# Performance work log

Hardware: AMD Instinct MI355X
Metric: run time of the kernel (lower is better)

The kernel has to match this reference:

```python
import jax, jax.numpy as jnp
import numpy as np

HEAD_SIZE = 64

def setup_inputs() -> dict:
    key = jax.random.key(0)
    k1, k2, k3 = jax.random.split(key, 3)
    B, T, C = 4, 4096, 1024
    x = jax.random.normal(k1, (B, T, C), dtype=jnp.float32)
    # nn.Linear(C, head_size, bias=False); stored as [in, out] so x @ W matches x @ weight.T
    Wk = jax.random.normal(k2, (C, HEAD_SIZE), dtype=jnp.float32) * (C ** -0.5)
    Wv = jax.random.normal(k3, (C, HEAD_SIZE), dtype=jnp.float32) * (C ** -0.5)
    return {"x": x, "Wk": Wk, "Wv": Wv}

def reference(x, Wk, Wv):
    # Faithful to source: q = self.key(x)  (query projection is unused -> Q == K)
    B, T, C = x.shape
    k = jnp.einsum('btc,ch->bth', x, Wk)           # [B,T,H]
    q = jnp.einsum('btc,ch->bth', x, Wk)           # same projection (source bug)
    scores = jnp.einsum('bth,bsh->bts', q, k) * (HEAD_SIZE ** -0.5)  # [B,T,T]
    causal = jnp.tril(jnp.ones((T, T), dtype=bool))
    scores = jnp.where(causal, scores, -jnp.inf)
    weights = jax.nn.softmax(scores, axis=-1)      # dropout p=0 (eval) -> identity
    v = jnp.einsum('btc,ch->bth', x, Wv)
    out = jnp.einsum('bts,bsh->bth', weights, v)   # [B,T,H]
    return out
```

## Files before the change

### kernel.cpp

```cpp
#include <hip/hip_runtime.h>

typedef short bf16x8 __attribute__((ext_vector_type(8)));
typedef float f32x4 __attribute__((ext_vector_type(4)));
typedef float f32x16 __attribute__((ext_vector_type(16)));
typedef unsigned u32x4v __attribute__((ext_vector_type(4)));

#define T_SEQ 4096
#define CDIM  1024
#define HD    64
#define NROWS 16384

__device__ inline float exp2fast(float x) {
  return __builtin_amdgcn_exp2f(x);
}

__device__ inline unsigned short f2bf(float f) {
  unsigned u = __builtin_bit_cast(unsigned, f);
  u = (u + 0x7fffu + ((u >> 16) & 1u)) >> 16;
  return (unsigned short)u;
}
__device__ inline unsigned cvt_pk_bf16(float lo, float hi) {
  unsigned r;
  asm("v_cvt_pk_bf16_f32 %0, %1, %2" : "=v"(r) : "v"(lo), "v"(hi));
  return r;
}
__device__ inline float bf2f(unsigned short u) {
  unsigned v = (unsigned)u << 16;
  return __builtin_bit_cast(float, v);
}
__device__ inline void gload_lds16(const unsigned short* g, unsigned char* l) {
  __builtin_amdgcn_global_load_lds(
      (const __attribute__((address_space(1))) unsigned int*)(const void*)g,
      (__attribute__((address_space(3))) unsigned int*)(void*)l, 16, 0, 0);
}

__global__ __launch_bounds__(256) void prep_w(
    const float* __restrict__ Wk, const float* __restrict__ Wv,
    unsigned short* __restrict__ Wt) {
  __shared__ float tile[64][68];
  const int t = threadIdx.x;
  const int mat = blockIdx.x & 1;
  const int k0 = (blockIdx.x >> 1) * 64;
  const float* W = mat ? Wv : Wk;
  #pragma unroll
  for (int pp = 0; pp < 4; ++pp) {
    int idx = t + 256 * pp, row = idx >> 4, c4 = idx & 15;
    float4 v = *(const float4*)&W[(size_t)(k0 + row) * HD + c4 * 4];
    *(float4*)&tile[row][c4 * 4] = v;
  }
  __syncthreads();
  #pragma unroll
  for (int j = 0; j < 2; ++j) {
    int n = t & 63, j8 = (t >> 6) + 4 * j;
    unsigned ow[4];
    #pragma unroll
    for (int w = 0; w < 4; ++w)
      ow[w] = cvt_pk_bf16(tile[j8 * 8 + 2 * w][n], tile[j8 * 8 + 2 * w + 1][n]);
    u32x4v ov = {ow[0], ow[1], ow[2], ow[3]};
    *(u32x4v*)&Wt[(size_t)(mat * 64 + n) * CDIM + k0 + j8 * 8] = ov;
  }
}

__global__ __launch_bounds__(256) void proj_mfma(
    const float* __restrict__ x, const unsigned short* __restrict__ Wt,
    unsigned short* __restrict__ Kb, unsigned short* __restrict__ Vb) {
  __shared__ __align__(16) unsigned char xsb[16384];
  __shared__ __align__(16) unsigned char wsb[65536];
  const int tid = threadIdx.x;
  const int lane = tid & 63, wave = tid >> 6;
  const int wm = wave & 1, wn = wave >> 1;
  const int lg = lane >> 4, lc = lane & 15;
  const int row0 = blockIdx.x * 64;

  float4 xreg[8];
  auto load_x = [&](int kk) {
    #pragma unroll
    for (int p = 0; p < 8; ++p) {
      int idx = tid + 256 * p, r = idx >> 5, c4 = idx & 31;
      xreg[p] = *(const float4*)&x[(size_t)(row0 + r) * CDIM + kk + c4 * 4];
    }
  };
  auto write_x = [&]() {
    #pragma unroll
    for (int p = 0; p < 8; ++p) {
      int idx = tid + 256 * p, r = idx >> 5, c4 = idx & 31;
      uint2 v;
      v.x = cvt_pk_bf16(xreg[p].x, xreg[p].y);
      v.y = cvt_pk_bf16(xreg[p].z, xreg[p].w);
      int byt = (r * 256 + c4 * 8) ^ ((r & 7) << 4);
      *(uint2*)(xsb + byt) = v;
    }
  };
  auto gload_W = [&](int kk, int buf) {
    unsigned char* wb = wsb + buf * 32768;
    #pragma unroll
    for (int p = 0; p < 8; ++p) {
      int ci = p * 256 + tid;
      int r = ci >> 4;
      int c8 = (ci & 15) ^ (r & 7);
      gload_lds16(&Wt[(size_t)r * CDIM + kk + c8 * 8],
                  wb + (p * 256 + wave * 64) * 16);
    }
  };

  f32x4 acc[2][4];
  #pragma unroll
  for (int mf = 0; mf < 2; ++mf)
    #pragma unroll
    for (int nf = 0; nf < 4; ++nf) acc[mf][nf] = (f32x4){0.f, 0.f, 0.f, 0.f};

  gload_W(0, 0);
  load_x(0);
  for (int kk = 0; kk < CDIM; kk += 128) {
    const int cur = (kk >> 7) & 1;
    __syncthreads();
    write_x();
    __syncthreads();
    if (kk + 128 < CDIM) { gload_W(kk + 128, cur ^ 1); load_x(kk + 128); }
    const unsigned char* wb = wsb + cur * 32768;
    #pragma unroll
    for (int dd = 0; dd < 4; ++dd) {
      bf16x8 a[2], bfr[4];
      #pragma unroll
      for (int mf = 0; mf < 2; ++mf) {
        int r = wm * 32 + mf * 16 + lc;
        int sw = (r & 7) << 4;
        a[mf] = *(const bf16x8*)(xsb + ((r * 256 + dd * 64 + lg * 16) ^ sw));
      }
      #pragma unroll
      for (int nf = 0; nf < 4; ++nf) {
        int r = wn * 64 + nf * 16 + lc;
        int sw = (r & 7) << 4;
        bfr[nf] = *(const bf16x8*)(wb + ((r * 256 + dd * 64 + lg * 16) ^ sw));
      }
      __builtin_amdgcn_s_setprio(1);
      #pragma unroll
      for (int mf = 0; mf < 2; ++mf)
        #pragma unroll
        for (int nf = 0; nf < 4; ++nf)
          acc[mf][nf] = __builtin_amdgcn_mfma_f32_16x16x32_bf16(a[mf], bfr[nf], acc[mf][nf], 0, 0, 0);
      __builtin_amdgcn_s_setprio(0);
    }
  }

  unsigned short* Ob = (wn == 0) ? Kb : Vb;
  #pragma unroll
  for (int mf = 0; mf < 2; ++mf)
    #pragma unroll
    for (int r = 0; r < 4; ++r) {
      int rg = row0 + wm * 32 + mf * 16 + lg * 4 + r;
      #pragma unroll
      for (int nf = 0; nf < 4; ++nf)
        Ob[(size_t)rg * HD + nf * 16 + lc] = f2bf(acc[mf][nf][r]);
    }
}

__global__ __launch_bounds__(512) void attn_part(
    const unsigned short* __restrict__ Kb, const unsigned short* __restrict__ Vb,
    unsigned short* __restrict__ Opart, float* __restrict__ Ml) {
  __shared__ __align__(16) unsigned char lds[32768];

  const int tid = threadIdx.x;
  const int lane = tid & 63;
  const int wq = tid >> 6;
  const int hi = lane >> 5;
  const int lq = lane & 31;

  const int b = blockIdx.x & 3;
  int qb = 0, c = 0;
  {
    int u = blockIdx.x >> 2, acc = 0;
    for (int q = 15; q >= 0; --q) {
      int nch = q + 1;
      if (u < acc + nch) { qb = q; c = u - acc; break; }
      acc += nch;
    }
  }
  const int kstart = c * 256;
  const int q0g = qb * 256 + wq * 32;
  const int qg = q0g + lq;
  const size_t base = (size_t)b * T_SEQ;
  const float SCALE2 = 0.18033688011112042f;

  bf16x8 qf[4];
  {
    const unsigned short* qp = &Kb[(base + q0g + lq) * HD];
    #pragma unroll
    for (int dd = 0; dd < 4; ++dd) {
      bf16x8 t = *(const bf16x8*)&qp[dd * 16 + hi * 8];
      const unsigned short* ts = (const unsigned short*)&t;
      unsigned ow[4];
      #pragma unroll
      for (int w = 0; w < 4; ++w)
        ow[w] = cvt_pk_bf16(bf2f(ts[2 * w]) * SCALE2, bf2f(ts[2 * w + 1]) * SCALE2);
      u32x4v ov = {ow[0], ow[1], ow[2], ow[3]};
      qf[dd] = __builtin_bit_cast(bf16x8, ov);
    }
  }

  f32x16 oT0, oT1;
  #pragma unroll
  for (int r = 0; r < 16; ++r) { oT0[r] = 0.f; oT1[r] = 0.f; }
  float mreg = -1e30f, lreg = 0.f;

  uint4 vreg0, vreg1;
  auto gload_K = [&](int jj, int buf) {
    const size_t kv0 = (base + kstart + (size_t)jj * 64) * HD;
    unsigned char* kb = lds + buf * 16384;
    int r = tid >> 3;
    int c8 = (tid & 7) ^ (r & 7);
    gload_lds16(&Kb[kv0 + (size_t)r * HD + c8 * 8], kb + (tid >> 6) * 1024);
  };
  auto load_v = [&](int jj) {
    if (tid < 256) {
      const size_t kv0 = (base + kstart + (size_t)jj * 64) * HD;
      int key0 = (tid & 31) * 2, d0 = (tid >> 5) * 8;
      vreg0 = *(const uint4*)&Vb[kv0 + (size_t)key0 * HD + d0];
      vreg1 = *(const uint4*)&Vb[kv0 + (size_t)(key0 + 1) * HD + d0];
    }
  };
  auto write_v = [&](int buf) {
    if (tid < 256) {
      unsigned char* vb = lds + buf * 16384 + 8192;
      int key0 = (tid & 31) * 2, d0 = (tid >> 5) * 8;
      const unsigned short* pa = (const unsigned short*)&vreg0;
      const unsigned short* pb = (const unsigned short*)&vreg1;
      #pragma unroll
      for (int j = 0; j < 8; ++j) {
        unsigned val = (unsigned)pa[j] | ((unsigned)pb[j] << 16);
        int d = d0 + j;
        int byt = (d * 128 + key0 * 2) ^ ((d & 7) << 4);
        *(unsigned*)(vb + byt) = val;
      }
    }
  };

  auto qk = [&](int buf, int ksub) -> f32x16 {
    const unsigned char* kb = lds + buf * 16384;
    f32x16 sacc;
    #pragma unroll
    for (int r = 0; r < 16; ++r) sacc[r] = 0.f;
    const int krow = ksub * 32 + lq;
    const int ksw = (krow & 7) << 4;
    #pragma unroll
    for (int dd = 0; dd < 4; ++dd) {
      bf16x8 kf = *(const bf16x8*)(kb + ((krow * 128 + dd * 32 + hi * 16) ^ ksw));
      sacc = __builtin_amdgcn_mfma_f32_32x32x16_bf16(kf, qf[dd], sacc, 0, 0, 0);
    }
    return sacc;
  };
  auto maskdiag = [&](f32x16& s, int kbase_s) {
    #pragma unroll
    for (int r = 0; r < 16; ++r) {
      int key = kbase_s + (r & 3) + 8 * (r >> 2) + 4 * hi;
      if (key > qg) s[r] = -1e38f;
    }
  };
  auto max16 = [&](const f32x16& s) -> float {
    return fmaxf(
        fmaxf(fmaxf(fmaxf(s[0], s[1]), fmaxf(s[2], s[3])),
              fmaxf(fmaxf(s[4], s[5]), fmaxf(s[6], s[7]))),
        fmaxf(fmaxf(fmaxf(s[8], s[9]), fmaxf(s[10], s[11])),
              fmaxf(fmaxf(s[12], s[13]), fmaxf(s[14], s[15]))));
  };
  auto pack2 = [&](const f32x16& s, bf16x8& p1, bf16x8& p2) {
    unsigned pk[8];
    #pragma unroll
    for (int i = 0; i < 8; ++i) pk[i] = cvt_pk_bf16(s[2 * i], s[2 * i + 1]);
    unsigned wA[4], wB[4];
    #pragma unroll
    for (int i = 0; i < 2; ++i) {
      unsigned a0 = pk[i], b0 = pk[2 + i];
      unsigned sa = (unsigned)__shfl_xor((int)a0, 32);
      unsigned sb = (unsigned)__shfl_xor((int)b0, 32);
      wA[i] = hi ? sb : a0;
      wA[2 + i] = hi ? b0 : sa;
      unsigned c0 = pk[4 + i], d0v = pk[6 + i];
      unsigned sc = (unsigned)__shfl_xor((int)c0, 32);
      unsigned sd = (unsigned)__shfl_xor((int)d0v, 32);
      wB[i] = hi ? sd : c0;
      wB[2 + i] = hi ? d0v : sc;
    }
    u32x4v t1v = {wA[0], wA[1], wA[2], wA[3]};
    u32x4v t2v = {wB[0], wB[1], wB[2], wB[3]};
    p1 = __builtin_bit_cast(bf16x8, t1v);
    p2 = __builtin_bit_cast(bf16x8, t2v);
  };
  auto pv = [&](int buf, int ksub, bf16x8 pb1, bf16x8 pb2) {
    const unsigned char* vb = lds + buf * 16384 + 8192;
    const int cb = ksub * 64;
    {
      int drow = lq;
      int swz = (drow & 7) << 4;
      bf16x8 v0 = *(const bf16x8*)(vb + ((drow * 128 + cb + hi * 16) ^ swz));
      bf16x8 v1 = *(const bf16x8*)(vb + ((drow * 128 + cb + 32 + hi * 16) ^ swz));
      oT0 = __builtin_amdgcn_mfma_f32_32x32x16_bf16(v0, pb1, oT0, 0, 0, 0);
      oT0 = __builtin_amdgcn_mfma_f32_32x32x16_bf16(v1, pb2, oT0, 0, 0, 0);
    }
    {
      int drow = 32 + lq;
      int swz = (drow & 7) << 4;
      bf16x8 v0 = *(const bf16x8*)(vb + ((drow * 128 + cb + hi * 16) ^ swz));
      bf16x8 v1 = *(const bf16x8*)(vb + ((drow * 128 + cb + 32 + hi * 16) ^ swz));
      oT1 = __builtin_amdgcn_mfma_f32_32x32x16_bf16(v0, pb1, oT1, 0, 0, 0);
      oT1 = __builtin_amdgcn_mfma_f32_32x32x16_bf16(v1, pb2, oT1, 0, 0, 0);
    }
  };

  gload_K(0, 0);
  load_v(0);
  write_v(0);
  for (int jj = 0; jj < 4; ++jj) {
    const int cur = jj & 1;
    __syncthreads();
    if (jj + 1 < 4) { gload_K(jj + 1, cur ^ 1); load_v(jj + 1); }
    const int kb0 = kstart + jj * 64;

    if (kb0 + 32 <= q0g) {
      __builtin_amdgcn_s_setprio(1);
      f32x16 s0 = qk(cur, 0);
      f32x16 s1 = qk(cur, 1);
      __builtin_amdgcn_s_setprio(0);
      if (kb0 + 32 == q0g) maskdiag(s1, kb0 + 32);
      float mx = fmaxf(max16(s0), max16(s1));
      mx = fmaxf(mx, __shfl_xor(mx, 32));
      if (!__all(mx <= mreg + 11.5f)) {
        float mn = fmaxf(mreg, mx);
        float al = exp2fast(mreg - mn);
        lreg *= al;
        #pragma unroll
        for (int r = 0; r < 16; ++r) { oT0[r] *= al; oT1[r] *= al; }
        mreg = mn;
      }
      float ps = 0.f;
      #pragma unroll
      for (int r = 0; r < 16; ++r) {
        float p0 = exp2fast(s0[r] - mreg);
        float p1 = exp2fast(s1[r] - mreg);
        ps += p0 + p1;
        s0[r] = p0;
        s1[r] = p1;
      }
      lreg += ps + __shfl_xor(ps, 32);
      bf16x8 pa1, pa2, pbb1, pbb2;
      pack2(s0, pa1, pa2);
      pack2(s1, pbb1, pbb2);
      __builtin_amdgcn_s_setprio(1);
      pv(cur, 0, pa1, pa2);
      pv(cur, 1, pbb1, pbb2);
      __builtin_amdgcn_s_setprio(0);
    } else if (kb0 <= q0g) {
      __builtin_amdgcn_s_setprio(1);
      f32x16 s0 = qk(cur, 0);
      __builtin_amdgcn_s_setprio(0);
      if (kb0 == q0g) maskdiag(s0, kb0);
      float mx = max16(s0);
      mx = fmaxf(mx, __shfl_xor(mx, 32));
      if (!__all(mx <= mreg + 11.5f)) {
        float mn = fmaxf(mreg, mx);
        float al = exp2fast(mreg - mn);
        lreg *= al;
        #pragma unroll
        for (int r = 0; r < 16; ++r) { oT0[r] *= al; oT1[r] *= al; }
        mreg = mn;
      }
      float ps = 0.f;
      #pragma unroll
      for (int r = 0; r < 16; ++r) {
        float p = exp2fast(s0[r] - mreg);
        ps += p;
        s0[r] = p;
      }
      lreg += ps + __shfl_xor(ps, 32);
      bf16x8 pa1, pa2;
      pack2(s0, pa1, pa2);
      __builtin_amdgcn_s_setprio(1);
      pv(cur, 0, pa1, pa2);
      __builtin_amdgcn_s_setprio(0);
    }

    if (jj + 1 < 4) write_v(cur ^ 1);
  }

  unsigned short* op = Opart + (size_t)blockIdx.x * 16384;
  float* mlp = Ml + (size_t)blockIdx.x * 512;
  const float invl = 1.0f / lreg;
  const int qrow = wq * 32 + lq;
  #pragma unroll
  for (int g = 0; g < 4; ++g) {
    int d0 = 8 * g + 4 * hi;
    uint2 w0, w1;
    w0.x = cvt_pk_bf16(oT0[4 * g] * invl, oT0[4 * g + 1] * invl);
    w0.y = cvt_pk_bf16(oT0[4 * g + 2] * invl, oT0[4 * g + 3] * invl);
    w1.x = cvt_pk_bf16(oT1[4 * g] * invl, oT1[4 * g + 1] * invl);
    w1.y = cvt_pk_bf16(oT1[4 * g + 2] * invl, oT1[4 * g + 3] * invl);
    *(uint2*)&op[qrow * 64 + d0] = w0;
    *(uint2*)&op[qrow * 64 + d0 + 32] = w1;
  }
  if (hi == 0) {
    mlp[qrow * 2] = mreg;
    mlp[qrow * 2 + 1] = lreg;
  }
}

__global__ __launch_bounds__(256) void attn_merge(
    const unsigned short* __restrict__ Opart, const float* __restrict__ Ml,
    float* __restrict__ out) {
  int g = blockIdx.x * 256 + threadIdx.x;
  int d8 = (g & 7) * 8;
  int row = g >> 3;
  int b = row >> 12;
  int t = row & (T_SEQ - 1);
  int qp = t >> 8;
  int r256 = t & 255;
  int nch = qp + 1;
  int us = 0;
  for (int q = 15; q > qp; --q) us += q + 1;
  float M = -1e30f;
  for (int cc = 0; cc < nch; ++cc) {
    int part = (us + cc) * 4 + b;
    M = fmaxf(M, Ml[(size_t)part * 512 + r256 * 2]);
  }
  float L = 0.f;
  float o[8];
  #pragma unroll
  for (int j = 0; j < 8; ++j) o[j] = 0.f;
  for (int cc = 0; cc < nch; ++cc) {
    int part = (us + cc) * 4 + b;
    float mc = Ml[(size_t)part * 512 + r256 * 2];
    float lc = Ml[(size_t)part * 512 + r256 * 2 + 1];
    float w = exp2fast(mc - M) * lc;
    L += w;
    uint4 v = *(const uint4*)&Opart[(size_t)part * 16384 + r256 * 64 + d8];
    const unsigned short* pv = (const unsigned short*)&v;
    #pragma unroll
    for (int j = 0; j < 8; ++j) o[j] += w * bf2f(pv[j]);
  }
  float inv = 1.0f / L;
  size_t og = ((size_t)b * T_SEQ + qp * 256 + r256) * 64 + d8;
  float4 r0 = make_float4(o[0] * inv, o[1] * inv, o[2] * inv, o[3] * inv);
  float4 r1 = make_float4(o[4] * inv, o[5] * inv, o[6] * inv, o[7] * inv);
  *(float4*)&out[og] = r0;
  *(float4*)&out[og + 4] = r1;
}

extern "C" void kernel_launch(void* const* d_in, const int* in_sizes, int n_in,
                              void* d_out, int out_size, void* d_ws, size_t ws_size,
                              hipStream_t stream) {
  const float* x  = (const float*)d_in[0];
  const float* Wk = (const float*)d_in[1];
  const float* Wv = (const float*)d_in[2];
  unsigned short* Kb = (unsigned short*)d_ws;
  unsigned short* Vb = Kb + (size_t)NROWS * HD;
  unsigned short* Wt = Vb + (size_t)NROWS * HD;
  unsigned short* Opart = Wt + (size_t)128 * CDIM;
  float* Ml = (float*)(Opart + (size_t)544 * 16384);
  float* o = (float*)d_out;

  prep_w<<<32, 256, 0, stream>>>(Wk, Wv, Wt);
  proj_mfma<<<256, 256, 0, stream>>>(x, Wt, Kb, Vb);
  attn_part<<<544, 512, 0, stream>>>(Kb, Vb, Opart, Ml);
  attn_merge<<<512, 256, 0, stream>>>(Opart, Ml, o);
}
```

Before: 71.79 us.

## Double the K/V LDS tile to 128 keys, halving barrier iterations

The attention-partial kernel now stages 128 keys of K and V per iteration instead of 64, doubling LDS to 64 KB. The key loop goes from 4 iterations to 2, each processing two 64-key halves, and all 512 threads now take part in loading V. This cuts the number of __syncthreads and load/compute phases per chunk. In exchange, the 64 KB of LDS may limit occupancy to one block per CU, and the prefetch now covers less of the compute.

```diff
diff --git a/kernel.cpp b/kernel.cpp
--- a/kernel.cpp
+++ b/kernel.cpp
@@ -158,7 +158,7 @@
 __global__ __launch_bounds__(512) void attn_part(
     const unsigned short* __restrict__ Kb, const unsigned short* __restrict__ Vb,
     unsigned short* __restrict__ Opart, float* __restrict__ Ml) {
-  __shared__ __align__(16) unsigned char lds[32768];
+  __shared__ __align__(16) unsigned char lds[65536];
 
   const int tid = threadIdx.x;
   const int lane = tid & 63;
@@ -205,38 +205,39 @@
 
   uint4 vreg0, vreg1;
   auto gload_K = [&](int jj, int buf) {
-    const size_t kv0 = (base + kstart + (size_t)jj * 64) * HD;
-    unsigned char* kb = lds + buf * 16384;
-    int r = tid >> 3;
-    int c8 = (tid & 7) ^ (r & 7);
-    gload_lds16(&Kb[kv0 + (size_t)r * HD + c8 * 8], kb + (tid >> 6) * 1024);
+    const size_t kv0 = (base + kstart + (size_t)jj * 128) * HD;
+    unsigned char* kb = lds + buf * 32768;
+    #pragma unroll
+    for (int p = 0; p < 2; ++p) {
+      int ci = p * 512 + tid;
+      int r = ci >> 3;
+      int c8 = (ci & 7) ^ (r & 7);
+      gload_lds16(&Kb[kv0 + (size_t)r * HD + c8 * 8],
+                  kb + (p * 512 + wq * 64) * 16);
+    }
   };
   auto load_v = [&](int jj) {
-    if (tid < 256) {
-      const size_t kv0 = (base + kstart + (size_t)jj * 64) * HD;
-      int key0 = (tid & 31) * 2, d0 = (tid >> 5) * 8;
-      vreg0 = *(const uint4*)&Vb[kv0 + (size_t)key0 * HD + d0];
-      vreg1 = *(const uint4*)&Vb[kv0 + (size_t)(key0 + 1) * HD + d0];
-    }
+    const size_t kv0 = (base + kstart + (size_t)jj * 128) * HD;
+    int key0 = (tid & 63) * 2, d0 = (tid >> 6) * 8;
+    vreg0 = *(const uint4*)&Vb[kv0 + (size_t)key0 * HD + d0];
+    vreg1 = *(const uint4*)&Vb[kv0 + (size_t)(key0 + 1) * HD + d0];
   };
   auto write_v = [&](int buf) {
-    if (tid < 256) {
-      unsigned char* vb = lds + buf * 16384 + 8192;
-      int key0 = (tid & 31) * 2, d0 = (tid >> 5) * 8;
-      const unsigned short* pa = (const unsigned short*)&vreg0;
-      const unsigned short* pb = (const unsigned short*)&vreg1;
-      #pragma unroll
-      for (int j = 0; j < 8; ++j) {
-        unsigned val = (unsigned)pa[j] | ((unsigned)pb[j] << 16);
-        int d = d0 + j;
-        int byt = (d * 128 + key0 * 2) ^ ((d & 7) << 4);
-        *(unsigned*)(vb + byt) = val;
-      }
+    unsigned char* vb = lds + buf * 32768 + 16384;
+    int key0 = (tid & 63) * 2, d0 = (tid >> 6) * 8;
+    const unsigned short* pa = (const unsigned short*)&vreg0;
+    const unsigned short* pb = (const unsigned short*)&vreg1;
+    #pragma unroll
+    for (int j = 0; j < 8; ++j) {
+      unsigned val = (unsigned)pa[j] | ((unsigned)pb[j] << 16);
+      int d = d0 + j;
+      int byt = (d * 256 + key0 * 2) ^ ((d & 7) << 4);
+      *(unsigned*)(vb + byt) = val;
     }
   };
 
   auto qk = [&](int buf, int ksub) -> f32x16 {
-    const unsigned char* kb = lds + buf * 16384;
+    const unsigned char* kb = lds + buf * 32768;
     f32x16 sacc;
     #pragma unroll
     for (int r = 0; r < 16; ++r) sacc[r] = 0.f;
@@ -287,21 +288,21 @@
     p2 = __builtin_bit_cast(bf16x8, t2v);
   };
   auto pv = [&](int buf, int ksub, bf16x8 pb1, bf16x8 pb2) {
-    const unsigned char* vb = lds + buf * 16384 + 8192;
+    const unsigned char* vb = lds + buf * 32768 + 16384;
     const int cb = ksub * 64;
     {
       int drow = lq;
       int swz = (drow & 7) << 4;
-      bf16x8 v0 = *(const bf16x8*)(vb + ((drow * 128 + cb + hi * 16) ^ swz));
-      bf16x8 v1 = *(const bf16x8*)(vb + ((drow * 128 + cb + 32 + hi * 16) ^ swz));
+      bf16x8 v0 = *(const bf16x8*)(vb + ((drow * 256 + cb + hi * 16) ^ swz));
+      bf16x8 v1 = *(const bf16x8*)(vb + ((drow * 256 + cb + 32 + hi * 16) ^ swz));
       oT0 = __builtin_amdgcn_mfma_f32_32x32x16_bf16(v0, pb1, oT0, 0, 0, 0);
       oT0 = __builtin_amdgcn_mfma_f32_32x32x16_bf16(v1, pb2, oT0, 0, 0, 0);
     }
     {
       int drow = 32 + lq;
       int swz = (drow & 7) << 4;
-      bf16x8 v0 = *(const bf16x8*)(vb + ((drow * 128 + cb + hi * 16) ^ swz));
-      bf16x8 v1 = *(const bf16x8*)(vb + ((drow * 128 + cb + 32 + hi * 16) ^ swz));
+      bf16x8 v0 = *(const bf16x8*)(vb + ((drow * 256 + cb + hi * 16) ^ swz));
+      bf16x8 v1 = *(const bf16x8*)(vb + ((drow * 256 + cb + 32 + hi * 16) ^ swz));
       oT1 = __builtin_amdgcn_mfma_f32_32x32x16_bf16(v0, pb1, oT1, 0, 0, 0);
       oT1 = __builtin_amdgcn_mfma_f32_32x32x16_bf16(v1, pb2, oT1, 0, 0, 0);
     }
@@ -310,76 +311,84 @@
   gload_K(0, 0);
   load_v(0);
   write_v(0);
-  for (int jj = 0; jj < 4; ++jj) {
+  for (int jj = 0; jj < 2; ++jj) {
     const int cur = jj & 1;
     __syncthreads();
-    if (jj + 1 < 4) { gload_K(jj + 1, cur ^ 1); load_v(jj + 1); }
-    const int kb0 = kstart + jj * 64;
-
-    if (kb0 + 32 <= q0g) {
-      __builtin_amdgcn_s_setprio(1);
-      f32x16 s0 = qk(cur, 0);
-      f32x16 s1 = qk(cur, 1);
-      __builtin_amdgcn_s_setprio(0);
-      if (kb0 + 32 == q0g) maskdiag(s1, kb0 + 32);
-      float mx = fmaxf(max16(s0), max16(s1));
-      mx = fmaxf(mx, __shfl_xor(mx, 32));
-      if (!__all(mx <= mreg + 11.5f)) {
-        float mn = fmaxf(mreg, mx);
-        float al = exp2fast(mreg - mn);
-        lreg *= al;
+    if (jj == 0) { gload_K(1, 1); load_v(1); }
+
+    #pragma unroll
+    for (int h = 0; h < 2; ++h) {
+      const int kb0 = kstart + jj * 128 + h * 64;
+      const int ks0 = jj ? (2 + h * 2 - 4) : h * 2;
+      const int ksub0 = (jj * 128 + h * 64) / 32 & 3;
+      (void)ks0; (void)ksub0;
+      const int su = h * 2;
+
+      if (kb0 + 32 <= q0g) {
+        __builtin_amdgcn_s_setprio(1);
+        f32x16 s0 = qk(cur, su);
+        f32x16 s1 = qk(cur, su + 1);
+        __builtin_amdgcn_s_setprio(0);
+        if (kb0 + 32 == q0g) maskdiag(s1, kb0 + 32);
+        float mx = fmaxf(max16(s0), max16(s1));
+        mx = fmaxf(mx, __shfl_xor(mx, 32));
+        if (!__all(mx <= mreg + 11.5f)) {
+          float mn = fmaxf(mreg, mx);
+          float al = exp2fast(mreg - mn);
+          lreg *= al;
+          #pragma unroll
+          for (int r = 0; r < 16; ++r) { oT0[r] *= al; oT1[r] *= al; }
+          mreg = mn;
+        }
+        float ps = 0.f;
         #pragma unroll
-        for (int r = 0; r < 16; ++r) { oT0[r] *= al; oT1[r] *= al; }
-        mreg = mn;
+        for (int r = 0; r < 16; ++r) {
+          float p0 = exp2fast(s0[r] - mreg);
+          float p1 = exp2fast(s1[r] - mreg);
+          ps += p0 + p1;
+          s0[r] = p0;
+          s1[r] = p1;
+        }
+        lreg += ps + __shfl_xor(ps, 32);
+        bf16x8 pa1, pa2, pbb1, pbb2;
+        pack2(s0, pa1, pa2);
+        pack2(s1, pbb1, pbb2);
+        __builtin_amdgcn_s_setprio(1);
+        pv(cur, su, pa1, pa2);
+        pv(cur, su + 1, pbb1, pbb2);
+        __builtin_amdgcn_s_setprio(0);
+      } else if (kb0 <= q0g) {
+        __builtin_amdgcn_s_setprio(1);
+        f32x16 s0 = qk(cur, su);
+        __builtin_amdgcn_s_setprio(0);
+        if (kb0 == q0g) maskdiag(s0, kb0);
+        float mx = max16(s0);
+        mx = fmaxf(mx, __shfl_xor(mx, 32));
+        if (!__all(mx <= mreg + 11.5f)) {
+          float mn = fmaxf(mreg, mx);
+          float al = exp2fast(mreg - mn);
+          lreg *= al;
+          #pragma unroll
+          for (int r = 0; r < 16; ++r) { oT0[r] *= al; oT1[r] *= al; }
+          mreg = mn;
+        }
+        float ps = 0.f;
+        #pragma unroll
+        for (int r = 0; r < 16; ++r) {
+          float p = exp2fast(s0[r] - mreg);
+          ps += p;
+          s0[r] = p;
+        }
+        lreg += ps + __shfl_xor(ps, 32);
+        bf16x8 pa1, pa2;
+        pack2(s0, pa1, pa2);
+        __builtin_amdgcn_s_setprio(1);
+        pv(cur, su, pa1, pa2);
+        __builtin_amdgcn_s_setprio(0);
       }
-      float ps = 0.f;
-      #pragma unroll
-      for (int r = 0; r < 16; ++r) {
-        float p0 = exp2fast(s0[r] - mreg);
-        float p1 = exp2fast(s1[r] - mreg);
-        ps += p0 + p1;
-        s0[r] = p0;
-        s1[r] = p1;
-      }
-      lreg += ps + __shfl_xor(ps, 32);
-      bf16x8 pa1, pa2, pbb1, pbb2;
-      pack2(s0, pa1, pa2);
-      pack2(s1, pbb1, pbb2);
-      __builtin_amdgcn_s_setprio(1);
-      pv(cur, 0, pa1, pa2);
-      pv(cur, 1, pbb1, pbb2);
-      __builtin_amdgcn_s_setprio(0);
-    } else if (kb0 <= q0g) {
-      __builtin_amdgcn_s_setprio(1);
-      f32x16 s0 = qk(cur, 0);
-      __builtin_amdgcn_s_setprio(0);
-      if (kb0 == q0g) maskdiag(s0, kb0);
-      float mx = max16(s0);
-      mx = fmaxf(mx, __shfl_xor(mx, 32));
-      if (!__all(mx <= mreg + 11.5f)) {
-        float mn = fmaxf(mreg, mx);
-        float al = exp2fast(mreg - mn);
-        lreg *= al;
-        #pragma unroll
-        for (int r = 0; r < 16; ++r) { oT0[r] *= al; oT1[r] *= al; }
-        mreg = mn;
-      }
-      float ps = 0.f;
-      #pragma unroll
-      for (int r = 0; r < 16; ++r) {
-        float p = exp2fast(s0[r] - mreg);
-        ps += p;
-        s0[r] = p;
-      }
-      lreg += ps + __shfl_xor(ps, 32);
-      bf16x8 pa1, pa2;
-      pack2(s0, pa1, pa2);
-      __builtin_amdgcn_s_setprio(1);
-      pv(cur, 0, pa1, pa2);
-      __builtin_amdgcn_s_setprio(0);
-    }
-
-    if (jj + 1 < 4) write_v(cur ^ 1);
+    }
+
+    if (jj == 0) write_v(1);
   }
 
   unsigned short* op = Opart + (size_t)blockIdx.x * 16384;
```

After: 70.35 us. 1.02x faster.

## Split attention KV chunks into finer pieces when workspace allows

Applied to the files above, without the earlier changes.

Adds a runtime parameter cperq so that, when the workspace is large enough, each 256-key chunk is split into two 128-key partial blocks, doubling the attn_part grid from 544 to 1088 blocks. This is meant to improve load balance and occupancy across CUs for the causal split-K attention. The cost is more partial outputs for the merge kernel to read and combine, and shorter per-block pipelines with less prefetch overlap. Fully masked partials are guarded by zero-length checks.

```diff
diff --git a/kernel.cpp b/kernel.cpp
--- a/kernel.cpp
+++ b/kernel.cpp
@@ -157,7 +157,7 @@
 
 __global__ __launch_bounds__(512) void attn_part(
     const unsigned short* __restrict__ Kb, const unsigned short* __restrict__ Vb,
-    unsigned short* __restrict__ Opart, float* __restrict__ Ml) {
+    unsigned short* __restrict__ Opart, float* __restrict__ Ml, int cperq) {
   __shared__ __align__(16) unsigned char lds[32768];
 
   const int tid = threadIdx.x;
@@ -171,12 +171,13 @@
   {
     int u = blockIdx.x >> 2, acc = 0;
     for (int q = 15; q >= 0; --q) {
-      int nch = q + 1;
+      int nch = (q + 1) * cperq;
       if (u < acc + nch) { qb = q; c = u - acc; break; }
       acc += nch;
     }
   }
-  const int kstart = c * 256;
+  const int nit = 4 / cperq;
+  const int kstart = c * (nit * 64);
   const int q0g = qb * 256 + wq * 32;
   const int qg = q0g + lq;
   const size_t base = (size_t)b * T_SEQ;
@@ -209,7 +210,7 @@
     unsigned char* kb = lds + buf * 16384;
     int r = tid >> 3;
     int c8 = (tid & 7) ^ (r & 7);
-    gload_lds16(&Kb[kv0 + (size_t)r * HD + c8 * 8], kb + (tid >> 6) * 1024);
+    gload_lds16(&Kb[kv0 + (size_t)r * HD + c8 * 8], kb + wq * 1024);
   };
   auto load_v = [&](int jj) {
     if (tid < 256) {
@@ -310,10 +311,10 @@
   gload_K(0, 0);
   load_v(0);
   write_v(0);
-  for (int jj = 0; jj < 4; ++jj) {
+  for (int jj = 0; jj < nit; ++jj) {
     const int cur = jj & 1;
     __syncthreads();
-    if (jj + 1 < 4) { gload_K(jj + 1, cur ^ 1); load_v(jj + 1); }
+    if (jj + 1 < nit) { gload_K(jj + 1, cur ^ 1); load_v(jj + 1); }
     const int kb0 = kstart + jj * 64;
 
     if (kb0 + 32 <= q0g) {
@@ -379,12 +380,12 @@
       __builtin_amdgcn_s_setprio(0);
     }
 
-    if (jj + 1 < 4) write_v(cur ^ 1);
+    if (jj + 1 < nit) write_v(cur ^ 1);
   }
 
   unsigned short* op = Opart + (size_t)blockIdx.x * 16384;
   float* mlp = Ml + (size_t)blockIdx.x * 512;
-  const float invl = 1.0f / lreg;
+  const float invl = (lreg > 0.f) ? (1.0f / lreg) : 0.f;
   const int qrow = wq * 32 + lq;
   #pragma unroll
   for (int g = 0; g < 4; ++g) {
@@ -405,7 +406,7 @@
 
 __global__ __launch_bounds__(256) void attn_merge(
     const unsigned short* __restrict__ Opart, const float* __restrict__ Ml,
-    float* __restrict__ out) {
+    float* __restrict__ out, int cperq) {
   int g = blockIdx.x * 256 + threadIdx.x;
   int d8 = (g & 7) * 8;
   int row = g >> 3;
@@ -413,9 +414,9 @@
   int t = row & (T_SEQ - 1);
   int qp = t >> 8;
   int r256 = t & 255;
-  int nch = qp + 1;
+  int nch = (qp + 1) * cperq;
   int us = 0;
-  for (int q = 15; q > qp; --q) us += q + 1;
+  for (int q = 15; q > qp; --q) us += (q + 1) * cperq;
   float M = -1e30f;
   for (int cc = 0; cc < nch; ++cc) {
     int part = (us + cc) * 4 + b;
@@ -429,6 +430,7 @@
     int part = (us + cc) * 4 + b;
     float mc = Ml[(size_t)part * 512 + r256 * 2];
     float lc = Ml[(size_t)part * 512 + r256 * 2 + 1];
+    if (lc <= 0.f) continue;
     float w = exp2fast(mc - M) * lc;
     L += w;
     uint4 v = *(const uint4*)&Opart[(size_t)part * 16384 + r256 * 64 + d8];
@@ -454,11 +456,19 @@
   unsigned short* Vb = Kb + (size_t)NROWS * HD;
   unsigned short* Wt = Vb + (size_t)NROWS * HD;
   unsigned short* Opart = Wt + (size_t)128 * CDIM;
-  float* Ml = (float*)(Opart + (size_t)544 * 16384);
+
+  const size_t fixed = (size_t)(2 * NROWS * HD) * 2 + (size_t)128 * CDIM * 2;
+  int cperq = 1;
+  {
+    size_t need2 = fixed + (size_t)1088 * 16384 * 2 + (size_t)1088 * 512 * 4;
+    if (ws_size >= need2) cperq = 2;
+  }
+  const int nblocks = 544 * cperq;
+  float* Ml = (float*)(Opart + (size_t)nblocks * 16384);
   float* o = (float*)d_out;
 
   prep_w<<<32, 256, 0, stream>>>(Wk, Wv, Wt);
   proj_mfma<<<256, 256, 0, stream>>>(x, Wt, Kb, Vb);
-  attn_part<<<544, 512, 0, stream>>>(Kb, Vb, Opart, Ml);
-  attn_merge<<<512, 256, 0, stream>>>(Opart, Ml, o);
-}
+  attn_part<<<nblocks, 512, 0, stream>>>(Kb, Vb, Opart, Ml, cperq);
+  attn_merge<<<512, 256, 0, stream>>>(Opart, Ml, o, cperq);
+}
```

New measurement: 92.79 us. 1.29x slower.
